# Kernel tuning notes

Measured on AMD Instinct MI355X. Metric: run time of the kernel, lower is better.

## Reference

```python
import jax, jax.numpy as jnp
import numpy as np

DIM = 1024
HID = 2048
E = 4

def setup_inputs() -> dict:
    key = jax.random.key(0)
    ks = jax.random.split(key, 7)
    s = lambda fan_in: 1.0 / np.sqrt(fan_in)
    x = jax.random.normal(ks[0], (2, 2048, DIM), dtype=jnp.float32)
    W1 = jax.random.uniform(ks[1], (E, DIM, HID), jnp.float32, -s(DIM), s(DIM))
    b1 = jax.random.uniform(ks[2], (E, HID), jnp.float32, -s(DIM), s(DIM))
    W2 = jax.random.uniform(ks[3], (E, HID, DIM), jnp.float32, -s(HID), s(HID))
    b2 = jax.random.uniform(ks[4], (E, DIM), jnp.float32, -s(HID), s(HID))
    Wr = jax.random.uniform(ks[5], (DIM, E), jnp.float32, -s(DIM), s(DIM))
    br = jax.random.uniform(ks[6], (E,), jnp.float32, -s(DIM), s(DIM))
    return {"x": x, "W1": W1, "b1": b1, "W2": W2, "b2": b2, "Wr": Wr, "br": br}

def reference(x, W1, b1, W2, b2, Wr, br):
    # router softmax weights: [B,T,E]
    weights = jax.nn.softmax(x @ Wr + br, axis=-1)
    # all-expert MLP: hidden [B,T,E,H]
    h = jax.nn.gelu(jnp.einsum('btd,edh->bteh', x, W1) + b1, approximate=False)
    # expert outputs [B,T,E,D]
    y = jnp.einsum('bteh,ehd->bted', h, W2) + b2
    # softmax-weighted combine over experts
    return jnp.einsum('bte,bted->btd', weights, y)
```

## Files before the change

### kernel.cpp

```cpp
#include <hip/hip_runtime.h>
#include <hip/hip_bf16.h>
#include <math.h>

#define DIM 1024
#define HID 2048
#define NE  4
#define NT  4096
#define KW  (NE*HID)
#define KSPLIT 2
#define KCH (KW / KSPLIT)

typedef __attribute__((ext_vector_type(8))) short short8;
typedef __attribute__((ext_vector_type(4))) short short4v;
typedef __attribute__((ext_vector_type(4))) float floatx4;


__device__ __forceinline__ void async_cp16(const void* g, void* l) {
  __builtin_amdgcn_global_load_lds(
      (const __attribute__((address_space(1))) void*)g,
      (__attribute__((address_space(3))) void*)l, 16, 0, 0);
}

__device__ __forceinline__ short f2bf(float f) {
  union { float f; unsigned u; } x; x.f = f;
  unsigned r = x.u + 0x7fffu + ((x.u >> 16) & 1u);
  return (short)(r >> 16);
}

__device__ __forceinline__ float gelu_fast(float v) {
  float u = 1.595769122f * (v + 0.044715f * v * v * v);
  return v * __builtin_amdgcn_rcpf(1.0f + __expf(-u));
}

__global__ void router_cvt(const float* __restrict__ x, const float* __restrict__ Wr,
                           const float* __restrict__ br, float* __restrict__ wgt,
                           short* __restrict__ xb) {
  const int wv = threadIdx.x >> 6, lane = threadIdx.x & 63;
  const int t = blockIdx.x * 4 + wv;
  const float* xr = x + (size_t)t * DIM;
  short* xo = xb + (size_t)t * DIM;
  float a0 = 0.f, a1 = 0.f, a2 = 0.f, a3 = 0.f;
  #pragma unroll
  for (int p = 0; p < 4; p++) {
    const int d = p * 256 + lane * 4;
    floatx4 v = *(const floatx4*)&xr[d];
    short4v o;
    #pragma unroll
    for (int j = 0; j < 4; j++) {
      o[j] = f2bf(v[j]);
      floatx4 wr = *(const floatx4*)&Wr[(d + j) * 4];
      a0 += v[j] * wr[0]; a1 += v[j] * wr[1];
      a2 += v[j] * wr[2]; a3 += v[j] * wr[3];
    }
    *(short4v*)&xo[d] = o;
  }
  #pragma unroll
  for (int off = 32; off; off >>= 1) {
    a0 += __shfl_down(a0, off);
    a1 += __shfl_down(a1, off);
    a2 += __shfl_down(a2, off);
    a3 += __shfl_down(a3, off);
  }
  a0 = __shfl(a0, 0); a1 = __shfl(a1, 0); a2 = __shfl(a2, 0); a3 = __shfl(a3, 0);
  float s0 = a0 + br[0], s1 = a1 + br[1], s2 = a2 + br[2], s3 = a3 + br[3];
  float m = fmaxf(fmaxf(s0, s1), fmaxf(s2, s3));
  float e0 = __expf(s0 - m), e1 = __expf(s1 - m), e2 = __expf(s2 - m), e3 = __expf(s3 - m);
  float inv = 1.f / (e0 + e1 + e2 + e3);
  float v = (lane == 0) ? e0 : (lane == 1) ? e1 : (lane == 2) ? e2 : e3;
  if (lane < 4) wgt[t * 4 + lane] = v * inv;
}

#define TP_PADR 136
__global__ void transpose_all(const float* __restrict__ W1, short* __restrict__ w1t,
                              const float* __restrict__ W2, short* __restrict__ w2t) {
  __shared__ __align__(16) short tile[32 * TP_PADR];
  const int b = blockIdx.x;
  const float* in; short* out; int R, C, xt, yt;
  if (b < 2048) {
    const int e = b >> 9, rem = b & 511;
    xt = rem & 63; yt = rem >> 6; R = DIM; C = HID;
    in = W1 + (size_t)e * DIM * HID; out = w1t + (size_t)e * DIM * HID;
  } else {
    const int rem = b - 2048;
    xt = rem & 31; yt = rem >> 5; R = KW; C = DIM;
    in = W2; out = w2t;
  }
  const int c0 = xt * 32, r0 = yt * 128;
  const int t = threadIdx.x;
  const int cin = (t & 7) * 4;
  const int rin = t >> 3;
  #pragma unroll
  for (int i = 0; i < 4; i++) {
    const int r = rin + i * 32;
    floatx4 v = *(const floatx4*)&in[(size_t)(r0 + r) * C + c0 + cin];
    #pragma unroll
    for (int j = 0; j < 4; j++)
      tile[(cin + j) * TP_PADR + r] = f2bf(v[j]);
  }
  __syncthreads();
  const int ct = t >> 3;
  #pragma unroll
  for (int i = 0; i < 2; i++) {
    const int rc = (t & 7) + 8 * i;
    short8 vv = *(const short8*)&tile[ct * TP_PADR + rc * 8];
    *(short8*)&out[(size_t)(c0 + ct) * R + r0 + rc * 8] = vv;
  }
}


__global__ __launch_bounds__(256, 2)
void gemm1_kernel(const short* __restrict__ xb, const short* __restrict__ w1t,
                  const float* __restrict__ b1, const float* __restrict__ wgt,
                  short* __restrict__ hw) {
  const int b = blockIdx.x;
  const int xcd = b & 7, slot = b >> 3;
  const int m_grp = xcd & 3, e_pair = xcd >> 1 & 2;
  const int n_idx = slot & 15, m_off = (slot >> 4) & 7, e_off = slot >> 7;
  const int e  = (xcd >> 2) * 2 + e_off;
  const int m0 = (m_grp * 8 + m_off) * 128;
  const int n0 = n_idx * 128;
  (void)e_pair;
  const int tid = threadIdx.x;
  const int lane = tid & 63;
  const int wv = tid >> 6;
  const int wm = (wv >> 1) * 64, wn = (wv & 1) * 64;
  const int quad = lane >> 4, lrow = lane & 15;
  const int sr  = tid >> 3;
  const int kof = ((tid & 7) ^ (sr & 7)) * 8;
  const int rkey = lrow & 7;

  __shared__ __align__(16) short As[128 * 64];
  __shared__ __align__(16) short Bs[128 * 64];

  const short* Ap = xb;
  const short* Bp = w1t + (size_t)e * HID * DIM;

  floatx4 acc[4][4];
  #pragma unroll
  for (int i = 0; i < 4; i++)
    #pragma unroll
    for (int j = 0; j < 4; j++) acc[i][j] = (floatx4)0.f;

  for (int k0 = 0; k0 < DIM; k0 += 64) {
    __syncthreads();
    #pragma unroll
    for (int c = 0; c < 4; c++)
      async_cp16(Ap + (size_t)(m0 + c * 32 + sr) * DIM + k0 + kof,
                 As + (c * 256 + tid) * 8);
    #pragma unroll
    for (int c = 0; c < 4; c++)
      async_cp16(Bp + (size_t)(n0 + c * 32 + sr) * DIM + k0 + kof,
                 Bs + (c * 256 + tid) * 8);
    __syncthreads();
    #pragma unroll
    for (int kk = 0; kk < 2; kk++) {
      short8 af[4], bf[4];
      const int ko = ((kk * 4 + quad) ^ rkey) * 8;
      #pragma unroll
      for (int i = 0; i < 4; i++)
        af[i] = *(const short8*)&As[(wm + i * 16 + lrow) * 64 + ko];
      #pragma unroll
      for (int j = 0; j < 4; j++)
        bf[j] = *(const short8*)&Bs[(wn + j * 16 + lrow) * 64 + ko];
      #pragma unroll
      for (int i = 0; i < 4; i++)
        #pragma unroll
        for (int j = 0; j < 4; j++)
          acc[i][j] = __builtin_amdgcn_mfma_f32_16x16x32_bf16(af[i], bf[j], acc[i][j], 0, 0, 0);
    }
  }

  #pragma unroll
  for (int i = 0; i < 4; i++) {
    const int rbase = m0 + wm + i * 16 + quad * 4;
    float wv4[4];
    #pragma unroll
    for (int r = 0; r < 4; r++) wv4[r] = wgt[(rbase + r) * NE + e];
    #pragma unroll
    for (int j = 0; j < 4; j++) {
      const int col = n0 + wn + j * 16 + lrow;
      const float b1v = b1[e * HID + col];
      #pragma unroll
      for (int r = 0; r < 4; r++) {
        float v = acc[i][j][r] + b1v;
        hw[(size_t)(rbase + r) * KW + e * HID + col] = f2bf(wv4[r] * gelu_fast(v));
      }
    }
  }
}

__global__ __launch_bounds__(256, 2)
void gemm2_kernel(const short* __restrict__ hw, const short* __restrict__ w2t,
                  const float* __restrict__ b2, const float* __restrict__ wgt,
                  float* __restrict__ out, float* __restrict__ part) {
  const int b = blockIdx.x;
  const int xcd = b & 7, slot = b >> 3;
  const int m_grp = xcd & 3, kz = xcd >> 2;
  const int n_idx = slot & 7, m_off = slot >> 3;
  const int m0 = (m_grp * 8 + m_off) * 128;
  const int n0 = n_idx * 128;
  const int tid = threadIdx.x;
  const int lane = tid & 63;
  const int wv = tid >> 6;
  const int wm = (wv >> 1) * 64, wn = (wv & 1) * 64;
  const int quad = lane >> 4, lrow = lane & 15;
  const int sr  = tid >> 3;
  const int kof = ((tid & 7) ^ (sr & 7)) * 8;
  const int rkey = lrow & 7;

  __shared__ __align__(16) short As[128 * 64];
  __shared__ __align__(16) short Bs[128 * 64];

  floatx4 acc[4][4];
  #pragma unroll
  for (int i = 0; i < 4; i++)
    #pragma unroll
    for (int j = 0; j < 4; j++) acc[i][j] = (floatx4)0.f;

  const int kbeg = kz * KCH;
  for (int kk0 = 0; kk0 < KCH; kk0 += 64) {
    const int k0 = kbeg + kk0;
    __syncthreads();
    #pragma unroll
    for (int c = 0; c < 4; c++)
      async_cp16(hw + (size_t)(m0 + c * 32 + sr) * KW + k0 + kof,
                 As + (c * 256 + tid) * 8);
    #pragma unroll
    for (int c = 0; c < 4; c++)
      async_cp16(w2t + (size_t)(n0 + c * 32 + sr) * KW + k0 + kof,
                 Bs + (c * 256 + tid) * 8);
    __syncthreads();
    #pragma unroll
    for (int kk = 0; kk < 2; kk++) {
      short8 af[4], bf[4];
      const int ko = ((kk * 4 + quad) ^ rkey) * 8;
      #pragma unroll
      for (int i = 0; i < 4; i++)
        af[i] = *(const short8*)&As[(wm + i * 16 + lrow) * 64 + ko];
      #pragma unroll
      for (int j = 0; j < 4; j++)
        bf[j] = *(const short8*)&Bs[(wn + j * 16 + lrow) * 64 + ko];
      #pragma unroll
      for (int i = 0; i < 4; i++)
        #pragma unroll
        for (int j = 0; j < 4; j++)
          acc[i][j] = __builtin_amdgcn_mfma_f32_16x16x32_bf16(af[i], bf[j], acc[i][j], 0, 0, 0);
    }
  }

  if (kz == 0) {
    #pragma unroll
    for (int i = 0; i < 4; i++) {
      const int rbase = m0 + wm + i * 16 + quad * 4;
      floatx4 wr[4];
      #pragma unroll
      for (int r = 0; r < 4; r++) wr[r] = *(const floatx4*)&wgt[(rbase + r) * NE];
      #pragma unroll
      for (int j = 0; j < 4; j++) {
        const int col = n0 + wn + j * 16 + lrow;
        float b2v[4];
        #pragma unroll
        for (int eI = 0; eI < 4; eI++) b2v[eI] = b2[eI * DIM + col];
        #pragma unroll
        for (int r = 0; r < 4; r++) {
          float bias = wr[r][0] * b2v[0] + wr[r][1] * b2v[1] +
                       wr[r][2] * b2v[2] + wr[r][3] * b2v[3];
          out[(size_t)(rbase + r) * DIM + col] = acc[i][j][r] + bias;
        }
      }
    }
  } else {
    #pragma unroll
    for (int i = 0; i < 4; i++) {
      const int rbase = m0 + wm + i * 16 + quad * 4;
      #pragma unroll
      for (int j = 0; j < 4; j++) {
        const int col = n0 + wn + j * 16 + lrow;
        #pragma unroll
        for (int r = 0; r < 4; r++)
          part[(size_t)(rbase + r) * DIM + col] = acc[i][j][r];
      }
    }
  }
}

__global__ void reduce_out(float* __restrict__ out, const float* __restrict__ part) {
  int i = (blockIdx.x * 256 + threadIdx.x) * 4;
  floatx4 v = *(const floatx4*)&out[i];
  floatx4 a = *(const floatx4*)&part[i];
  v = v + a;
  *(floatx4*)&out[i] = v;
}


extern "C" void kernel_launch(void* const* d_in, const int* in_sizes, int n_in,
                              void* d_out, int out_size, void* d_ws, size_t ws_size,
                              hipStream_t stream) {
  const float* x  = (const float*)d_in[0];
  const float* W1 = (const float*)d_in[1];
  const float* b1 = (const float*)d_in[2];
  const float* W2 = (const float*)d_in[3];
  const float* b2 = (const float*)d_in[4];
  const float* Wr = (const float*)d_in[5];
  const float* br = (const float*)d_in[6];
  float* out = (float*)d_out;

  char* ws = (char*)d_ws;
  float* wgt = (float*)(ws);
  short* w2t = (short*)(ws + 65536);
  short* hw  = (short*)(ws + 65536 + 16777216);
  short* xb  = (short*)(ws + 65536 + 16777216 + 67108864);
  short* w1t = (short*)(ws + 65536 + 16777216 + 67108864 + 8388608);
  float* part= (float*)(ws + 65536 + 16777216 + 67108864);

  hipLaunchKernelGGL(router_cvt, dim3(NT / 4), dim3(256), 0, stream, x, Wr, br, wgt, xb);
  hipLaunchKernelGGL(transpose_all, dim3(2048 + 2048), dim3(256), 0, stream,
                     W1, w1t, W2, w2t);
  hipLaunchKernelGGL(gemm1_kernel, dim3(2048), dim3(256), 0, stream,
                     xb, w1t, b1, wgt, hw);
  hipLaunchKernelGGL(gemm2_kernel, dim3(512), dim3(256), 0, stream,
                     hw, w2t, b2, wgt, out, part);
  hipLaunchKernelGGL(reduce_out, dim3(NT * DIM / 1024), dim3(256), 0, stream, out, part);
}
```

Baseline: 285.6 us.

## Pipeline both GEMMs with 4-stage async LDS ring and larger tiles

Rewrites gemm1 and gemm2 main loops to use a 4-slot LDS ring buffer filled by async global-to-LDS copies, with vmcnt-based waits plus a single barrier per K-step replacing the two syncthreads per iteration. Block size grows to 512 threads, with gemm1 tiles at 256x256 and gemm2 at 256x128. The K-step shrinks to 32 and the LDS swizzle is redesigned for it, and setprio is raised around MFMA bursts. This is meant to hide global load latency and raise data reuse, at the cost of much more LDS per block (128KB for gemm1), which may cut occupancy, and of fewer blocks per grid.

```diff
diff --git a/kernel.cpp b/kernel.cpp
--- a/kernel.cpp
+++ b/kernel.cpp
@@ -31,6 +31,11 @@
   float u = 1.595769122f * (v + 0.044715f * v * v * v);
   return v * __builtin_amdgcn_rcpf(1.0f + __expf(-u));
 }
+
+#define WBAR(N) do { \
+    asm volatile("s_waitcnt vmcnt(" #N ")" ::: "memory"); \
+    __builtin_amdgcn_s_barrier(); \
+  } while (0)
 
 __global__ void router_cvt(const float* __restrict__ x, const float* __restrict__ Wr,
                            const float* __restrict__ br, float* __restrict__ wgt,
@@ -108,108 +113,118 @@
 }
 
 
-__global__ __launch_bounds__(256, 2)
+__global__ __launch_bounds__(512, 2)
 void gemm1_kernel(const short* __restrict__ xb, const short* __restrict__ w1t,
                   const float* __restrict__ b1, const float* __restrict__ wgt,
                   short* __restrict__ hw) {
+  __shared__ __align__(16) short lds[65536];
   const int b = blockIdx.x;
   const int xcd = b & 7, slot = b >> 3;
-  const int m_grp = xcd & 3, e_pair = xcd >> 1 & 2;
-  const int n_idx = slot & 15, m_off = (slot >> 4) & 7, e_off = slot >> 7;
-  const int e  = (xcd >> 2) * 2 + e_off;
-  const int m0 = (m_grp * 8 + m_off) * 128;
-  const int n0 = n_idx * 128;
-  (void)e_pair;
+  const int m0 = ((xcd & 3) * 4 + (slot & 3)) * 256;
+  const int n0 = ((xcd >> 2) * 16 + (slot >> 2)) * 256;
   const int tid = threadIdx.x;
-  const int lane = tid & 63;
-  const int wv = tid >> 6;
-  const int wm = (wv >> 1) * 64, wn = (wv & 1) * 64;
+  const int lane = tid & 63, wv = tid >> 6;
+  const int wm = (wv >> 2) * 128, wn = (wv & 3) * 64;
   const int quad = lane >> 4, lrow = lane & 15;
-  const int sr  = tid >> 3;
-  const int kof = ((tid & 7) ^ (sr & 7)) * 8;
-  const int rkey = lrow & 7;
-
-  __shared__ __align__(16) short As[128 * 64];
-  __shared__ __align__(16) short Bs[128 * 64];
-
-  const short* Ap = xb;
-  const short* Bp = w1t + (size_t)e * HID * DIM;
-
-  floatx4 acc[4][4];
-  #pragma unroll
-  for (int i = 0; i < 4; i++)
+
+  const int srow = tid >> 3, su = (tid & 7) ^ (srow & 7);
+  const int sm = 2 * srow + (su >> 2), skc = su & 3;
+  const short* srcA0 = xb + (size_t)(m0 + sm) * DIM + skc * 8;
+  const short* srcA1 = srcA0 + (size_t)128 * DIM;
+  const short* srcB0 = w1t + (size_t)(n0 + sm) * DIM + skc * 8;
+  const short* srcB1 = srcB0 + (size_t)128 * DIM;
+
+  const int cswz = (quad | ((lrow & 1) << 2)) ^ (lrow >> 1);
+  const int offA = ((wm >> 1) + (lrow >> 1)) * 64 + cswz * 8;
+  const int offB = ((wn >> 1) + (lrow >> 1)) * 64 + cswz * 8;
+
+  floatx4 acc[8][4];
+  #pragma unroll
+  for (int i = 0; i < 8; i++)
     #pragma unroll
     for (int j = 0; j < 4; j++) acc[i][j] = (floatx4)0.f;
 
-  for (int k0 = 0; k0 < DIM; k0 += 64) {
-    __syncthreads();
-    #pragma unroll
-    for (int c = 0; c < 4; c++)
-      async_cp16(Ap + (size_t)(m0 + c * 32 + sr) * DIM + k0 + kof,
-                 As + (c * 256 + tid) * 8);
-    #pragma unroll
-    for (int c = 0; c < 4; c++)
-      async_cp16(Bp + (size_t)(n0 + c * 32 + sr) * DIM + k0 + kof,
-                 Bs + (c * 256 + tid) * 8);
-    __syncthreads();
-    #pragma unroll
-    for (int kk = 0; kk < 2; kk++) {
-      short8 af[4], bf[4];
-      const int ko = ((kk * 4 + quad) ^ rkey) * 8;
-      #pragma unroll
-      for (int i = 0; i < 4; i++)
-        af[i] = *(const short8*)&As[(wm + i * 16 + lrow) * 64 + ko];
-      #pragma unroll
-      for (int j = 0; j < 4; j++)
-        bf[j] = *(const short8*)&Bs[(wn + j * 16 + lrow) * 64 + ko];
-      #pragma unroll
-      for (int i = 0; i < 4; i++)
-        #pragma unroll
-        for (int j = 0; j < 4; j++)
-          acc[i][j] = __builtin_amdgcn_mfma_f32_16x16x32_bf16(af[i], bf[j], acc[i][j], 0, 0, 0);
-    }
-  }
-
-  #pragma unroll
-  for (int i = 0; i < 4; i++) {
+#define G1_STAGE(sl, tk) do { \
+    short* Ab = &lds[(sl) * 8192]; short* Bb = &lds[32768 + (sl) * 8192]; \
+    async_cp16(srcA0 + (tk) * 32, Ab + tid * 8); \
+    async_cp16(srcA1 + (tk) * 32, Ab + 4096 + tid * 8); \
+    async_cp16(srcB0 + (tk) * 32, Bb + tid * 8); \
+    async_cp16(srcB1 + (tk) * 32, Bb + 4096 + tid * 8); \
+  } while (0)
+
+#define G1_COMP(sl) do { \
+    const short* Ab = &lds[(sl) * 8192]; const short* Bb = &lds[32768 + (sl) * 8192]; \
+    short8 af[8], bfr[4]; \
+    _Pragma("unroll") for (int i = 0; i < 8; i++) \
+      af[i] = *(const short8*)&Ab[offA + i * 512]; \
+    _Pragma("unroll") for (int j = 0; j < 4; j++) \
+      bfr[j] = *(const short8*)&Bb[offB + j * 512]; \
+    __builtin_amdgcn_s_setprio(1); \
+    _Pragma("unroll") for (int i = 0; i < 8; i++) \
+      _Pragma("unroll") for (int j = 0; j < 4; j++) \
+        acc[i][j] = __builtin_amdgcn_mfma_f32_16x16x32_bf16(af[i], bfr[j], acc[i][j], 0, 0, 0); \
+    __builtin_amdgcn_s_setprio(0); \
+  } while (0)
+
+  G1_STAGE(0, 0);
+  G1_STAGE(1, 1);
+  for (int t = 0; t < 28; t += 4) {
+    G1_STAGE(2, t + 2); WBAR(8); G1_COMP(0);
+    G1_STAGE(3, t + 3); WBAR(8); G1_COMP(1);
+    G1_STAGE(0, t + 4); WBAR(8); G1_COMP(2);
+    G1_STAGE(1, t + 5); WBAR(8); G1_COMP(3);
+  }
+  G1_STAGE(2, 30); WBAR(8); G1_COMP(0);
+  G1_STAGE(3, 31); WBAR(8); G1_COMP(1);
+  WBAR(4); G1_COMP(2);
+  WBAR(0); G1_COMP(3);
+#undef G1_STAGE
+#undef G1_COMP
+
+  const int e = n0 >> 11;
+  #pragma unroll
+  for (int i = 0; i < 8; i++) {
     const int rbase = m0 + wm + i * 16 + quad * 4;
-    float wv4[4];
-    #pragma unroll
-    for (int r = 0; r < 4; r++) wv4[r] = wgt[(rbase + r) * NE + e];
+    float w4[4];
+    #pragma unroll
+    for (int r = 0; r < 4; r++) w4[r] = wgt[(rbase + r) * NE + e];
     #pragma unroll
     for (int j = 0; j < 4; j++) {
       const int col = n0 + wn + j * 16 + lrow;
-      const float b1v = b1[e * HID + col];
+      const float b1v = b1[e * HID + (col & (HID - 1))];
       #pragma unroll
       for (int r = 0; r < 4; r++) {
         float v = acc[i][j][r] + b1v;
-        hw[(size_t)(rbase + r) * KW + e * HID + col] = f2bf(wv4[r] * gelu_fast(v));
+        hw[(size_t)(rbase + r) * KW + col] = f2bf(w4[r] * gelu_fast(v));
       }
     }
   }
 }
 
-__global__ __launch_bounds__(256, 2)
+__global__ __launch_bounds__(512, 2)
 void gemm2_kernel(const short* __restrict__ hw, const short* __restrict__ w2t,
                   const float* __restrict__ b2, const float* __restrict__ wgt,
                   float* __restrict__ out, float* __restrict__ part) {
+  __shared__ __align__(16) short lds[49152];
   const int b = blockIdx.x;
   const int xcd = b & 7, slot = b >> 3;
-  const int m_grp = xcd & 3, kz = xcd >> 2;
-  const int n_idx = slot & 7, m_off = slot >> 3;
-  const int m0 = (m_grp * 8 + m_off) * 128;
-  const int n0 = n_idx * 128;
+  const int kz = xcd >> 2;
+  const int m0 = ((xcd & 3) * 4 + (slot & 3)) * 256;
+  const int n0 = (slot >> 2) * 128;
   const int tid = threadIdx.x;
-  const int lane = tid & 63;
-  const int wv = tid >> 6;
+  const int lane = tid & 63, wv = tid >> 6;
   const int wm = (wv >> 1) * 64, wn = (wv & 1) * 64;
   const int quad = lane >> 4, lrow = lane & 15;
-  const int sr  = tid >> 3;
-  const int kof = ((tid & 7) ^ (sr & 7)) * 8;
-  const int rkey = lrow & 7;
-
-  __shared__ __align__(16) short As[128 * 64];
-  __shared__ __align__(16) short Bs[128 * 64];
+
+  const int srow = tid >> 3, su = (tid & 7) ^ (srow & 7);
+  const int sm = 2 * srow + (su >> 2), skc = su & 3;
+  const short* srcA0 = hw + (size_t)(m0 + sm) * KW + kz * KCH + skc * 8;
+  const short* srcA1 = srcA0 + (size_t)128 * KW;
+  const short* srcB0 = w2t + (size_t)(n0 + sm) * KW + kz * KCH + skc * 8;
+
+  const int cswz = (quad | ((lrow & 1) << 2)) ^ (lrow >> 1);
+  const int offA = ((wm >> 1) + (lrow >> 1)) * 64 + cswz * 8;
+  const int offB = ((wn >> 1) + (lrow >> 1)) * 64 + cswz * 8;
 
   floatx4 acc[4][4];
   #pragma unroll
@@ -217,36 +232,41 @@
     #pragma unroll
     for (int j = 0; j < 4; j++) acc[i][j] = (floatx4)0.f;
 
-  const int kbeg = kz * KCH;
-  for (int kk0 = 0; kk0 < KCH; kk0 += 64) {
-    const int k0 = kbeg + kk0;
-    __syncthreads();
-    #pragma unroll
-    for (int c = 0; c < 4; c++)
-      async_cp16(hw + (size_t)(m0 + c * 32 + sr) * KW + k0 + kof,
-                 As + (c * 256 + tid) * 8);
-    #pragma unroll
-    for (int c = 0; c < 4; c++)
-      async_cp16(w2t + (size_t)(n0 + c * 32 + sr) * KW + k0 + kof,
-                 Bs + (c * 256 + tid) * 8);
-    __syncthreads();
-    #pragma unroll
-    for (int kk = 0; kk < 2; kk++) {
-      short8 af[4], bf[4];
-      const int ko = ((kk * 4 + quad) ^ rkey) * 8;
-      #pragma unroll
-      for (int i = 0; i < 4; i++)
-        af[i] = *(const short8*)&As[(wm + i * 16 + lrow) * 64 + ko];
-      #pragma unroll
-      for (int j = 0; j < 4; j++)
-        bf[j] = *(const short8*)&Bs[(wn + j * 16 + lrow) * 64 + ko];
-      #pragma unroll
-      for (int i = 0; i < 4; i++)
-        #pragma unroll
-        for (int j = 0; j < 4; j++)
-          acc[i][j] = __builtin_amdgcn_mfma_f32_16x16x32_bf16(af[i], bf[j], acc[i][j], 0, 0, 0);
-    }
-  }
+#define G2_STAGE(sl, tk) do { \
+    short* Ab = &lds[(sl) * 8192]; short* Bb = &lds[32768 + (sl) * 4096]; \
+    async_cp16(srcA0 + (tk) * 32, Ab + tid * 8); \
+    async_cp16(srcA1 + (tk) * 32, Ab + 4096 + tid * 8); \
+    async_cp16(srcB0 + (tk) * 32, Bb + tid * 8); \
+  } while (0)
+
+#define G2_COMP(sl) do { \
+    const short* Ab = &lds[(sl) * 8192]; const short* Bb = &lds[32768 + (sl) * 4096]; \
+    short8 af[4], bfr[4]; \
+    _Pragma("unroll") for (int i = 0; i < 4; i++) \
+      af[i] = *(const short8*)&Ab[offA + i * 512]; \
+    _Pragma("unroll") for (int j = 0; j < 4; j++) \
+      bfr[j] = *(const short8*)&Bb[offB + j * 512]; \
+    __builtin_amdgcn_s_setprio(1); \
+    _Pragma("unroll") for (int i = 0; i < 4; i++) \
+      _Pragma("unroll") for (int j = 0; j < 4; j++) \
+        acc[i][j] = __builtin_amdgcn_mfma_f32_16x16x32_bf16(af[i], bfr[j], acc[i][j], 0, 0, 0); \
+    __builtin_amdgcn_s_setprio(0); \
+  } while (0)
+
+  G2_STAGE(0, 0);
+  G2_STAGE(1, 1);
+  for (int t = 0; t < 124; t += 4) {
+    G2_STAGE(2, t + 2); WBAR(6); G2_COMP(0);
+    G2_STAGE(3, t + 3); WBAR(6); G2_COMP(1);
+    G2_STAGE(0, t + 4); WBAR(6); G2_COMP(2);
+    G2_STAGE(1, t + 5); WBAR(6); G2_COMP(3);
+  }
+  G2_STAGE(2, 126); WBAR(6); G2_COMP(0);
+  G2_STAGE(3, 127); WBAR(6); G2_COMP(1);
+  WBAR(3); G2_COMP(2);
+  WBAR(0); G2_COMP(3);
+#undef G2_STAGE
+#undef G2_COMP
 
   if (kz == 0) {
     #pragma unroll
@@ -316,9 +336,9 @@
   hipLaunchKernelGGL(router_cvt, dim3(NT / 4), dim3(256), 0, stream, x, Wr, br, wgt, xb);
   hipLaunchKernelGGL(transpose_all, dim3(2048 + 2048), dim3(256), 0, stream,
                      W1, w1t, W2, w2t);
-  hipLaunchKernelGGL(gemm1_kernel, dim3(2048), dim3(256), 0, stream,
+  hipLaunchKernelGGL(gemm1_kernel, dim3(512), dim3(512), 0, stream,
                      xb, w1t, b1, wgt, hw);
-  hipLaunchKernelGGL(gemm2_kernel, dim3(512), dim3(256), 0, stream,
+  hipLaunchKernelGGL(gemm2_kernel, dim3(256), dim3(512), 0, stream,
                      hw, w2t, b2, wgt, out, part);
   hipLaunchKernelGGL(reduce_out, dim3(NT * DIM / 1024), dim3(256), 0, stream, out, part);
 }
```

New measurement: 280.2 us. Within noise of the previous version (-1.9%).
